# Kernel optimization log

Hardware: AMD Instinct MI355X
Metric: run time of the kernel (lower is better)

The kernel has to match this reference:

```python
import math
import jax, jax.numpy as jnp
import numpy as np

# Module config (init_kwargs)
GRID = (11, 16, 24)          # (T, H, W) latent grid, T odd so T-1 == 2*(T//2)
POOL = 128                   # pool_size / block size
SPARSITY = 0.9
TXT_LEN = 384                # txt_len, txt_first=False
HEADS, HDIM = 8, 128
FFL = GRID[1] * GRID[2]      # first_frame_len = H*W = 384
SEQ = GRID[0] * FFL + TXT_LEN  # 4608 tokens, 36 blocks of 128


def _rearr(t):
    # rearrange_with_remaining, h%8==0 and w%8==0 path.
    # t: [b, (f h w), n, d] with f = T-1 frames (first frame excluded)
    b, s, n, d = t.shape
    T, H, W = GRID
    fn, hn, wn = T // 2, H // 8, W // 8
    x = t.transpose(0, 2, 1, 3).reshape(b * n, fn, 2, hn, 8, wn, 8, d)
    # 'b (fn fb)(hn hb)(wn wb) d -> b (fn hn wn fb hb wb) d'
    x = x.transpose(0, 1, 3, 5, 2, 4, 6, 7).reshape(b * n, s, d)
    return x.reshape(b, n, s, d).transpose(0, 2, 1, 3)


def _inv_rearr(t):
    b, s, n, d = t.shape
    T, H, W = GRID
    fn, hn, wn = T // 2, H // 8, W // 8
    x = t.transpose(0, 2, 1, 3).reshape(b * n, fn, hn, wn, 2, 8, 8, d)
    x = x.transpose(0, 1, 4, 2, 5, 3, 6, 7).reshape(b * n, s, d)
    return x.reshape(b, n, s, d).transpose(0, 2, 1, 3)


def _avgpool(t):
    # seq divisible by POOL -> mean over each block (tail branch unused)
    b, s, n, d = t.shape
    return t.reshape(b, s // POOL, POOL, n, d).mean(axis=2)


def _forward(q, k, v):
    b, s, n, d = q.shape
    scale = jnp.asarray(d, q.dtype) ** -0.5
    # do_tensor_rearrange_pooling on concatenated qkv (txt_first=False)
    qkv = jnp.concatenate([q, k, v], axis=0)
    f_part = qkv[:, :FFL]
    i_part = qkv[:, FFL:s - TXT_LEN]
    t_part = qkv[:, s - TXT_LEN:]
    qkv2 = jnp.concatenate([_rearr(i_part), f_part, t_part], axis=1)
    pool = _avgpool(qkv2)
    q2, k2, v2 = jnp.split(qkv2, 3, axis=0)
    qp, kp, _ = jnp.split(pool, 3, axis=0)
    # pooled block scores + softmax
    ps = jax.nn.softmax(jnp.einsum('blnd,bsnd->bnls', qp, kp) * scale, axis=-1)
    nb = s // POOL
    keep = math.ceil(nb * (1.0 - SPARSITY))
    thr = jax.lax.top_k(ps, keep)[0][..., -1:]
    mask = ps >= thr                              # [B, n, nb, nb] bool
    prot = (FFL + TXT_LEN + POOL - 1) // POOL
    mask = mask.at[:, :, -prot:, :].set(True)
    mask = mask.at[:, :, :, -prot:].set(True)
    bm = mask[0]                                  # [n, nb, nb] per-head block mask (batch 0, as kernel uses)
    tok = jnp.repeat(jnp.repeat(bm, POOL, axis=1), POOL, axis=2)  # [n, S, S]
    # block-sparse attention == masked dense attention over selected kv blocks
    scores = jnp.einsum('bqnd,bknd->bnqk', q2, k2) * scale
    scores = jnp.where(tok[None], scores, jnp.asarray(-1e30, scores.dtype))
    p = jax.nn.softmax(scores, axis=-1)
    x = jnp.einsum('bnqk,bknd->bqnd', p, v2)
    # do_tensor_inv_rearrange (txt_first=False: concat(f, i, t))
    si = s - TXT_LEN - FFL
    xi = _inv_rearr(x[:, :si])
    xf = x[:, si:si + FFL]
    xt = x[:, si + FFL:]
    return jnp.concatenate([xf, xi, xt], axis=1)


def setup_inputs() -> dict:
    key = jax.random.key(0)
    kq, kk, kv = jax.random.split(key, 3)
    q = jax.random.normal(kq, (1, SEQ, HEADS, HDIM), dtype=jnp.float32)
    k = jax.random.normal(kk, (1, SEQ, HEADS, HDIM), dtype=jnp.float32)
    v = jax.random.normal(kv, (1, SEQ, HEADS, HDIM), dtype=jnp.float32)
    t_b_idx = jnp.arange(2, dtype=jnp.int64 if jax.config.jax_enable_x64 else jnp.int32)
    return {'q': q, 'k': k, 'v': v, 't_b_idx': t_b_idx}


def reference(q, k, v, t_b_idx):
    # t_idx = t_b_idx[0] = 0, skip_timesteps = 0 -> sparse branch (static)
    return _forward(q, k, v)
```

## Files before the change

kernel.cpp:

```cpp
#include <hip/hip_runtime.h>


typedef __attribute__((ext_vector_type(8))) _Float16 half8;
typedef __attribute__((ext_vector_type(4))) _Float16 half4;
typedef __attribute__((ext_vector_type(4))) float float4v;

#define KROW 136
#define VROW 72
#define PPROW 40

__device__ __forceinline__ int orig_pos(int j) {
    if (j >= 3840) return (j < 4224) ? (j - 3840) : j;
    int blk = j >> 7;
    int r   = j & 127;
    int f   = blk / 6;
    int rem = blk - f * 6;
    int b2  = rem / 3;
    int e   = rem - b2 * 3;
    int a   = r >> 6;
    int c   = (r >> 3) & 7;
    int g   = r & 7;
    return 384 + (f * 2 + a) * 384 + (b2 * 8 + c) * 24 + e * 8 + g;
}

__device__ __forceinline__ void cp16(const void* g, void* l) {
    __builtin_amdgcn_global_load_lds((const __attribute__((address_space(1))) void*)g,
                                     (__attribute__((address_space(3))) void*)l, 16, 0, 0);
}

__global__ __launch_bounds__(256) void prep_kernel(const float* __restrict__ q,
                                                   const float* __restrict__ k,
                                                   const float* __restrict__ v,
                                                   short* __restrict__ Kc,
                                                   unsigned* __restrict__ Vt32,
                                                   float* __restrict__ qp,
                                                   float* __restrict__ kp) {
    __shared__ short Vs[64 * KROW];
    __shared__ float Rs[8 * 128];
    int bx  = blockIdx.x;
    int tid = threadIdx.x;

    if (bx < 576) {
        int sub = bx & 1;
        int kb  = (bx >> 1) % 36;
        int h   = bx / 72;

        int lr = tid >> 3;
        int ld = (tid & 7) << 2;
#pragma unroll
        for (int pass = 0; pass < 2; ++pass) {
            int lt  = pass * 32 + lr;
            int tok = sub * 64 + lt;
            int op  = orig_pos(kb * 128 + tok);
            const float* kr = k + ((size_t)op * 8 + h) * 128;
            const float* vr = v + ((size_t)op * 8 + h) * 128;
            short* ko = Kc + ((size_t)(h * 36 + kb) * 128 + tok) * KROW;
#pragma unroll
            for (int j = 0; j < 4; ++j) {
                int d = ld + j * 32;
                float4v xk = *reinterpret_cast<const float4v*>(kr + d);
                float4v xv = *reinterpret_cast<const float4v*>(vr + d);
                half4 hk, hv;
#pragma unroll
                for (int i = 0; i < 4; ++i) { hk[i] = (_Float16)xk[i]; hv[i] = (_Float16)xv[i]; }
                *reinterpret_cast<half4*>(ko + d) = hk;
                *reinterpret_cast<half4*>(&Vs[lt * KROW + d]) = hv;
            }
        }
        __syncthreads();

        {
            const unsigned short* Vsu = (const unsigned short*)Vs;
            unsigned* vo = Vt32 + (size_t)((h * 36 + kb) * 2 + sub) * 128 * (VROW / 2);
#pragma unroll
            for (int it = 0; it < 16; ++it) {
                int i   = it * 256 + tid;
                int tw  = i & 31;
                int dim = i >> 5;
                unsigned lo = Vsu[(2 * tw) * KROW + dim];
                unsigned hi = Vsu[(2 * tw + 1) * KROW + dim];
                vo[dim * (VROW / 2) + tw] = (hi << 16) | lo;
            }
        }
    } else {
        int bx2 = bx - 576;
        int sub = bx2 & 1;
        int kb  = (bx2 >> 1) % 36;
        int h   = bx2 / 72;

        const float* arr = sub ? q : k;
        int dq = (tid & 31) << 2;
        int g  = tid >> 5;
        float4v acc = {0.f, 0.f, 0.f, 0.f};
#pragma unroll
        for (int it = 0; it < 16; ++it) {
            int t  = g + it * 8;
            int op = orig_pos(kb * 128 + t);
            float4v x = *reinterpret_cast<const float4v*>(arr + ((size_t)op * 8 + h) * 128 + dq);
            acc[0] += x[0]; acc[1] += x[1]; acc[2] += x[2]; acc[3] += x[3];
        }
#pragma unroll
        for (int i = 0; i < 4; ++i) Rs[g * 128 + dq + i] = acc[i];
        __syncthreads();

        if (tid < 128) {
            float s = 0.f;
#pragma unroll
            for (int g2 = 0; g2 < 8; ++g2) s += Rs[g2 * 128 + tid];
            float* outp = sub ? qp : kp;
            outp[(h * 36 + kb) * 128 + tid] = s * (1.f / 128.f);
        }
    }
}

__global__ __launch_bounds__(256, 3) void flash_kernel(const float* __restrict__ q,
                                                       const short* __restrict__ Kc,
                                                       const short* __restrict__ Vt,
                                                       const float* __restrict__ qp,
                                                       const float* __restrict__ kp,
                                                       float* __restrict__ out,
                                                       float* __restrict__ pO,
                                                       float* __restrict__ pL) {
    __shared__ __align__(16) short Ks[64 * KROW];
    __shared__ __align__(16) short Vsh[128 * VROW];
    __shared__ __align__(16) short Ph[4 * 32 * PPROW];
    __shared__ int Ls[40];
    __shared__ float Lf[64];

    int t = blockIdx.x;
    int h, qb, half, nkb = 0, kbase = 0, pidx = -1;
    if (t < 288) {
        h = t & 7;
        int rest = t >> 3;
        int qbh = rest / 6, r2 = rest % 6;
        half = r2 / 3;
        int chunk = r2 % 3;
        qb = 30 + qbh; nkb = 12; kbase = chunk * 12; pidx = t;
    } else {
        int t2 = t - 288;
        h = t2 & 7;
        int rest = t2 >> 3;
        qb = rest >> 1; half = rest & 1;
    }

    int tid = threadIdx.x, wave = tid >> 6, lane = tid & 63;
    int m16 = lane & 15, quad = lane >> 4;
    int rh = wave & 1, th = wave >> 1;

    constexpr float kScale = 0.08838834764831845f * 1.4426950408889634f;

    half8 aq[2][4];
#pragma unroll
    for (int rg = 0; rg < 2; ++rg) {
        int qrow_frag = qb * 128 + half * 64 + rh * 32 + rg * 16 + m16;
        const float* qrp = q + ((size_t)orig_pos(qrow_frag) * 8 + h) * 128;
#pragma unroll
        for (int kc = 0; kc < 4; ++kc) {
            float4v x0 = *reinterpret_cast<const float4v*>(qrp + kc * 32 + quad * 8);
            float4v x1 = *reinterpret_cast<const float4v*>(qrp + kc * 32 + quad * 8 + 4);
#pragma unroll
            for (int j = 0; j < 4; ++j) {
                aq[rg][kc][j]     = (_Float16)(x0[j] * kScale);
                aq[rg][kc][4 + j] = (_Float16)(x1[j] * kScale);
            }
        }
    }

    if (pidx < 0 && wave == 0) {
        float s = -1e30f;
        if (lane < 36) {
            const float4v* qv = (const float4v*)(qp + (h * 36 + qb) * 128);
            const float4v* kv = (const float4v*)(kp + (h * 36 + lane) * 128);
            float acc = 0.f;
            for (int i = 0; i < 32; ++i) {
                float4v a = qv[i], b = kv[i];
                acc += a[0] * b[0] + a[1] * b[1] + a[2] * b[2] + a[3] * b[3];
            }
            s = acc;
        }
        float tmp = s;
        float thr = 0.f;
        for (int i = 0; i < 4; ++i) {
            float mx = tmp;
            for (int off = 1; off < 64; off <<= 1) mx = fmaxf(mx, __shfl_xor(mx, off));
            thr = mx;
            unsigned long long bal = __ballot(tmp == mx);
            int low = __ffsll(bal) - 1;
            if (lane == low) tmp = -3e38f;
        }
        bool keep = (lane < 36) && ((s >= thr) || (lane >= 30));
        unsigned long long mk = __ballot(keep);
        if (lane == 0) Ls[0] = __popcll(mk);
        if (keep) {
            int pos = __popcll(mk & ((1ull << lane) - 1ull));
            Ls[1 + pos] = lane;
        }
    }
    __syncthreads();
    if (pidx < 0) nkb = Ls[0];

    float l_r[2][4];
    float4v o[2][8];
#pragma unroll
    for (int rg = 0; rg < 2; ++rg) {
#pragma unroll
        for (int r = 0; r < 4; ++r) l_r[rg][r] = 0.f;
#pragma unroll
        for (int dt = 0; dt < 8; ++dt) { o[rg][dt][0] = 0.f; o[rg][dt][1] = 0.f; o[rg][dt][2] = 0.f; o[rg][dt][3] = 0.f; }
    }

    short* Phw = Ph + wave * (32 * PPROW);

    int ntile = nkb * 2;
    for (int it = 0; it < ntile; ++it) {
        int kb  = (pidx >= 0) ? (kbase + (it >> 1)) : Ls[1 + (it >> 1)];
        int sub = it & 1;
        const char* gK = (const char*)(Kc + ((size_t)((h * 36 + kb) * 128) + sub * 64) * KROW);
        const char* gV = (const char*)(Vt + (size_t)((h * 36 + kb) * 2 + sub) * 128 * VROW);

        __syncthreads();
        {
            char* lK = (char*)Ks;
            char* lV = (char*)Vsh;
            int off = lane * 16;
            for (int c = wave; c < 35; c += 4) {
                if (c < 17) cp16(gK + c * 1024 + off, lK + c * 1024 + off);
                else        cp16(gV + (c - 17) * 1024 + off, lV + (c - 17) * 1024 + off);
            }
        }
        __syncthreads();

        float4v sacc[2][2];
#pragma unroll
        for (int rg = 0; rg < 2; ++rg)
#pragma unroll
            for (int nt = 0; nt < 2; ++nt) { sacc[rg][nt][0] = 0.f; sacc[rg][nt][1] = 0.f; sacc[rg][nt][2] = 0.f; sacc[rg][nt][3] = 0.f; }
#pragma unroll
        for (int nt = 0; nt < 2; ++nt)
#pragma unroll
            for (int kc = 0; kc < 4; ++kc) {
                half8 bk = *reinterpret_cast<const half8*>(&Ks[(th * 32 + nt * 16 + m16) * KROW + kc * 32 + quad * 8]);
                sacc[0][nt] = __builtin_amdgcn_mfma_f32_16x16x32_f16(aq[0][kc], bk, sacc[0][nt], 0, 0, 0);
                sacc[1][nt] = __builtin_amdgcn_mfma_f32_16x16x32_f16(aq[1][kc], bk, sacc[1][nt], 0, 0, 0);
            }

#pragma unroll
        for (int rg = 0; rg < 2; ++rg)
#pragma unroll
            for (int r = 0; r < 4; ++r) {
                float p0 = exp2f(sacc[rg][0][r]);
                float p1 = exp2f(sacc[rg][1][r]);
                sacc[rg][0][r] = p0; sacc[rg][1][r] = p1;
                l_r[rg][r] += p0 + p1;
            }

#pragma unroll
        for (int rg = 0; rg < 2; ++rg)
#pragma unroll
            for (int nt = 0; nt < 2; ++nt)
#pragma unroll
                for (int r = 0; r < 4; ++r) {
                    union { _Float16 hf; short s; } cv;
                    cv.hf = (_Float16)sacc[rg][nt][r];
                    Phw[(rg * 16 + quad * 4 + r) * PPROW + nt * 16 + m16] = cv.s;
                }
        half8 ap[2];
#pragma unroll
        for (int rg = 0; rg < 2; ++rg)
            ap[rg] = *reinterpret_cast<const half8*>(&Phw[(rg * 16 + m16) * PPROW + quad * 8]);

#pragma unroll
        for (int dt = 0; dt < 8; ++dt) {
            half8 bv = *reinterpret_cast<const half8*>(&Vsh[(dt * 16 + m16) * VROW + th * 32 + quad * 8]);
            o[0][dt] = __builtin_amdgcn_mfma_f32_16x16x32_f16(ap[0], bv, o[0][dt], 0, 0, 0);
            o[1][dt] = __builtin_amdgcn_mfma_f32_16x16x32_f16(ap[1], bv, o[1][dt], 0, 0, 0);
        }
    }

#pragma unroll
    for (int rg = 0; rg < 2; ++rg)
#pragma unroll
        for (int r = 0; r < 4; ++r)
            for (int sh = 1; sh < 16; sh <<= 1) l_r[rg][r] += __shfl_xor(l_r[rg][r], sh);

    __syncthreads();
    {
        float* red = rh ? (float*)Vsh : (float*)Ks;
        if (th == 1) {
#pragma unroll
            for (int rg = 0; rg < 2; ++rg) {
#pragma unroll
                for (int dt = 0; dt < 8; ++dt)
#pragma unroll
                    for (int r = 0; r < 4; ++r)
                        red[(rg * 16 + quad * 4 + r) * 132 + dt * 16 + m16] = o[rg][dt][r];
                if (m16 == 0)
#pragma unroll
                    for (int r = 0; r < 4; ++r)
                        Lf[rh * 32 + rg * 16 + quad * 4 + r] = l_r[rg][r];
            }
        }
        __syncthreads();
        if (th == 0) {
#pragma unroll
            for (int rg = 0; rg < 2; ++rg)
#pragma unroll
                for (int dt = 0; dt < 8; ++dt)
#pragma unroll
                    for (int r = 0; r < 4; ++r)
                        o[rg][dt][r] += red[(rg * 16 + quad * 4 + r) * 132 + dt * 16 + m16];

            if (pidx >= 0) {
                float* po = pO + (size_t)pidx * 8192;
#pragma unroll
                for (int rg = 0; rg < 2; ++rg)
#pragma unroll
                    for (int r = 0; r < 4; ++r) {
                        int row = rh * 32 + rg * 16 + quad * 4 + r;
                        float lt2 = l_r[rg][r] + Lf[row];
#pragma unroll
                        for (int dt = 0; dt < 8; ++dt)
                            po[row * 128 + dt * 16 + m16] = o[rg][dt][r];
                        if (m16 == 0) pL[pidx * 64 + row] = lt2;
                    }
            } else {
#pragma unroll
                for (int rg = 0; rg < 2; ++rg)
#pragma unroll
                    for (int r = 0; r < 4; ++r) {
                        int row = rh * 32 + rg * 16 + quad * 4 + r;
                        int qrow = qb * 128 + half * 64 + row;
                        size_t base = ((size_t)orig_pos(qrow) * 8 + h) * 128;
                        float inv = 1.f / (l_r[rg][r] + Lf[row]);
#pragma unroll
                        for (int dt = 0; dt < 8; ++dt)
                            out[base + dt * 16 + m16] = o[rg][dt][r] * inv;
                    }
            }
        }
    }
}

__global__ void combine_kernel(const float* __restrict__ pO, const float* __restrict__ pL,
                               float* __restrict__ out) {
    int gb = blockIdx.x;
    int g  = gb >> 3;
    int rg = gb & 7;
    int h    = g / 12;
    int rem  = g % 12;
    int qbh  = rem >> 1;
    int half = rem & 1;
    int qb   = 30 + qbh;
    int base_t = (qbh * 6 + half * 3) * 8 + h;

    int tid = threadIdx.x;
    int d   = tid & 127;
    int r0  = tid >> 7;
#pragma unroll
    for (int itr = 0; itr < 4; ++itr) {
        int row = rg * 8 + r0 + itr * 2;
        float l = pL[(base_t + 0) * 64 + row] + pL[(base_t + 8) * 64 + row] + pL[(base_t + 16) * 64 + row];
        float acc = pO[(size_t)(base_t + 0) * 8192 + row * 128 + d]
                  + pO[(size_t)(base_t + 8) * 8192 + row * 128 + d]
                  + pO[(size_t)(base_t + 16) * 8192 + row * 128 + d];
        int qrow = qb * 128 + half * 64 + row;
        out[((size_t)orig_pos(qrow) * 8 + h) * 128 + d] = acc / l;
    }
}

extern "C" void kernel_launch(void* const* d_in, const int* in_sizes, int n_in,
                              void* d_out, int out_size, void* d_ws, size_t ws_size,
                              hipStream_t stream) {
    const float* q = (const float*)d_in[0];
    const float* k = (const float*)d_in[1];
    const float* v = (const float*)d_in[2];
    float* out = (float*)d_out;

    char* w = (char*)d_ws;
    short* Kc  = (short*)(w);
    short* Vt  = (short*)(w + 10027008);
    float* qp  = (float*)(w + 20643840);
    float* kp  = (float*)(w + 20791296);
    float* pL  = (float*)(w + 20938752);
    float* pO  = (float*)(w + 21012480);

    prep_kernel<<<dim3(1152), dim3(256), 0, stream>>>(q, k, v, Kc, (unsigned*)Vt, qp, kp);
    flash_kernel<<<dim3(768), dim3(256), 0, stream>>>(q, Kc, Vt, qp, kp, out, pO, pL);
    combine_kernel<<<dim3(768), dim3(256), 0, stream>>>(pO, pL, out);
}
```

Measured before the change: 169.7 us.

## Fuse K pooling into K/V conversion kernel and split Q pooling out

The K block-mean is now accumulated while K is converted to fp16, so K is no longer re-read from global memory by separate pooling blocks. Per-half partial sums are written and summed inside the flash kernel's block-selection step. The fp16 K tile is now staged in LDS and written out with coalesced 16-byte stores, and the V staging row is padded to 138 to cut LDS bank conflicts on the transpose. Q pooling moves into its own kernel launch, adding one launch of overhead. The mean scaling is dropped, which leaves the scores scaled by a positive constant and so keeps the same ordering.

Result: no change. 172.4 us (+1.6%).

```diff
diff --git a/kernel.cpp b/kernel.cpp
--- a/kernel.cpp
+++ b/kernel.cpp
@@ -3,10 +3,12 @@
 
 typedef __attribute__((ext_vector_type(8))) _Float16 half8;
 typedef __attribute__((ext_vector_type(4))) _Float16 half4;
+typedef __attribute__((ext_vector_type(2))) _Float16 half2v;
 typedef __attribute__((ext_vector_type(4))) float float4v;
 
 #define KROW 136
 #define VROW 72
+#define VSROW 138
 #define PPROW 40
 
 __device__ __forceinline__ int orig_pos(int j) {
@@ -28,88 +30,112 @@
                                      (__attribute__((address_space(3))) void*)l, 16, 0, 0);
 }
 
-__global__ __launch_bounds__(256) void prep_kernel(const float* __restrict__ q,
-                                                   const float* __restrict__ k,
+__global__ __launch_bounds__(256) void conv_kernel(const float* __restrict__ k,
                                                    const float* __restrict__ v,
                                                    short* __restrict__ Kc,
                                                    unsigned* __restrict__ Vt32,
-                                                   float* __restrict__ qp,
-                                                   float* __restrict__ kp) {
-    __shared__ short Vs[64 * KROW];
+                                                   float* __restrict__ kpart) {
+    __shared__ __align__(16) short KsL[64 * KROW];
+    __shared__ short VsL[64 * VSROW];
+    __shared__ float Rs[32 * 128];
+    int bx  = blockIdx.x;
+    int tid = threadIdx.x;
+    int sub = bx & 1;
+    int kb  = (bx >> 1) % 36;
+    int h   = bx / 72;
+
+    int lr  = tid >> 3;
+    int ld4 = (tid & 7) << 2;
+
+    float ksum[16];
+#pragma unroll
+    for (int i = 0; i < 16; ++i) ksum[i] = 0.f;
+
+#pragma unroll
+    for (int pass = 0; pass < 2; ++pass) {
+        int lt  = pass * 32 + lr;
+        int tok = sub * 64 + lt;
+        int op  = orig_pos(kb * 128 + tok);
+        const float* kr = k + ((size_t)op * 8 + h) * 128;
+        const float* vr = v + ((size_t)op * 8 + h) * 128;
+#pragma unroll
+        for (int j = 0; j < 4; ++j) {
+            int d = ld4 + j * 32;
+            float4v xk = *reinterpret_cast<const float4v*>(kr + d);
+            float4v xv = *reinterpret_cast<const float4v*>(vr + d);
+            half4 hk;
+            half2v hv0, hv1;
+#pragma unroll
+            for (int i = 0; i < 4; ++i) { hk[i] = (_Float16)xk[i]; ksum[j * 4 + i] += xk[i]; }
+            hv0[0] = (_Float16)xv[0]; hv0[1] = (_Float16)xv[1];
+            hv1[0] = (_Float16)xv[2]; hv1[1] = (_Float16)xv[3];
+            *reinterpret_cast<half4*>(&KsL[lt * KROW + d]) = hk;
+            *reinterpret_cast<half2v*>(&VsL[lt * VSROW + d]) = hv0;
+            *reinterpret_cast<half2v*>(&VsL[lt * VSROW + d + 2]) = hv1;
+        }
+    }
+#pragma unroll
+    for (int j = 0; j < 4; ++j)
+#pragma unroll
+        for (int i = 0; i < 4; ++i)
+            Rs[lr * 128 + ld4 + j * 32 + i] = ksum[j * 4 + i];
+    __syncthreads();
+
+    {
+        const float4v* src = reinterpret_cast<const float4v*>(KsL);
+        float4v* dst = reinterpret_cast<float4v*>(Kc + ((size_t)((h * 36 + kb) * 128) + sub * 64) * KROW);
+        for (int i = tid; i < 1088; i += 256) dst[i] = src[i];
+    }
+
+    {
+        const unsigned short* Vsu = (const unsigned short*)VsL;
+        unsigned* vo = Vt32 + (size_t)((h * 36 + kb) * 2 + sub) * 128 * (VROW / 2);
+#pragma unroll
+        for (int it = 0; it < 16; ++it) {
+            int i   = it * 256 + tid;
+            int tw  = i & 31;
+            int dim = i >> 5;
+            unsigned lo = Vsu[(2 * tw) * VSROW + dim];
+            unsigned hi = Vsu[(2 * tw + 1) * VSROW + dim];
+            vo[dim * (VROW / 2) + tw] = (hi << 16) | lo;
+        }
+    }
+
+    if (tid < 128) {
+        float s = 0.f;
+#pragma unroll
+        for (int g = 0; g < 32; ++g) s += Rs[g * 128 + tid];
+        kpart[(size_t)((h * 36 + kb) * 2 + sub) * 128 + tid] = s;
+    }
+}
+
+__global__ __launch_bounds__(256) void poolq_kernel(const float* __restrict__ q,
+                                                    float* __restrict__ qp) {
     __shared__ float Rs[8 * 128];
     int bx  = blockIdx.x;
     int tid = threadIdx.x;
-
-    if (bx < 576) {
-        int sub = bx & 1;
-        int kb  = (bx >> 1) % 36;
-        int h   = bx / 72;
-
-        int lr = tid >> 3;
-        int ld = (tid & 7) << 2;
-#pragma unroll
-        for (int pass = 0; pass < 2; ++pass) {
-            int lt  = pass * 32 + lr;
-            int tok = sub * 64 + lt;
-            int op  = orig_pos(kb * 128 + tok);
-            const float* kr = k + ((size_t)op * 8 + h) * 128;
-            const float* vr = v + ((size_t)op * 8 + h) * 128;
-            short* ko = Kc + ((size_t)(h * 36 + kb) * 128 + tok) * KROW;
-#pragma unroll
-            for (int j = 0; j < 4; ++j) {
-                int d = ld + j * 32;
-                float4v xk = *reinterpret_cast<const float4v*>(kr + d);
-                float4v xv = *reinterpret_cast<const float4v*>(vr + d);
-                half4 hk, hv;
-#pragma unroll
-                for (int i = 0; i < 4; ++i) { hk[i] = (_Float16)xk[i]; hv[i] = (_Float16)xv[i]; }
-                *reinterpret_cast<half4*>(ko + d) = hk;
-                *reinterpret_cast<half4*>(&Vs[lt * KROW + d]) = hv;
-            }
-        }
-        __syncthreads();
-
-        {
-            const unsigned short* Vsu = (const unsigned short*)Vs;
-            unsigned* vo = Vt32 + (size_t)((h * 36 + kb) * 2 + sub) * 128 * (VROW / 2);
-#pragma unroll
-            for (int it = 0; it < 16; ++it) {
-                int i   = it * 256 + tid;
-                int tw  = i & 31;
-                int dim = i >> 5;
-                unsigned lo = Vsu[(2 * tw) * KROW + dim];
-                unsigned hi = Vsu[(2 * tw + 1) * KROW + dim];
-                vo[dim * (VROW / 2) + tw] = (hi << 16) | lo;
-            }
-        }
-    } else {
-        int bx2 = bx - 576;
-        int sub = bx2 & 1;
-        int kb  = (bx2 >> 1) % 36;
-        int h   = bx2 / 72;
-
-        const float* arr = sub ? q : k;
-        int dq = (tid & 31) << 2;
-        int g  = tid >> 5;
-        float4v acc = {0.f, 0.f, 0.f, 0.f};
-#pragma unroll
-        for (int it = 0; it < 16; ++it) {
-            int t  = g + it * 8;
-            int op = orig_pos(kb * 128 + t);
-            float4v x = *reinterpret_cast<const float4v*>(arr + ((size_t)op * 8 + h) * 128 + dq);
-            acc[0] += x[0]; acc[1] += x[1]; acc[2] += x[2]; acc[3] += x[3];
-        }
-#pragma unroll
-        for (int i = 0; i < 4; ++i) Rs[g * 128 + dq + i] = acc[i];
-        __syncthreads();
-
-        if (tid < 128) {
-            float s = 0.f;
-#pragma unroll
-            for (int g2 = 0; g2 < 8; ++g2) s += Rs[g2 * 128 + tid];
-            float* outp = sub ? qp : kp;
-            outp[(h * 36 + kb) * 128 + tid] = s * (1.f / 128.f);
-        }
+    int kb  = bx % 36;
+    int h   = bx / 36;
+
+    int dq = (tid & 31) << 2;
+    int g  = tid >> 5;
+    float4v acc = {0.f, 0.f, 0.f, 0.f};
+#pragma unroll
+    for (int it = 0; it < 16; ++it) {
+        int t  = g + it * 8;
+        int op = orig_pos(kb * 128 + t);
+        float4v x = *reinterpret_cast<const float4v*>(q + ((size_t)op * 8 + h) * 128 + dq);
+        acc[0] += x[0]; acc[1] += x[1]; acc[2] += x[2]; acc[3] += x[3];
+    }
+#pragma unroll
+    for (int i = 0; i < 4; ++i) Rs[g * 128 + dq + i] = acc[i];
+    __syncthreads();
+
+    if (tid < 128) {
+        float s = 0.f;
+#pragma unroll
+        for (int g2 = 0; g2 < 8; ++g2) s += Rs[g2 * 128 + tid];
+        qp[(h * 36 + kb) * 128 + tid] = s;
     }
 }
 
@@ -117,7 +143,7 @@
                                                        const short* __restrict__ Kc,
                                                        const short* __restrict__ Vt,
                                                        const float* __restrict__ qp,
-                                                       const float* __restrict__ kp,
+                                                       const float* __restrict__ kpart,
                                                        float* __restrict__ out,
                                                        float* __restrict__ pO,
                                                        float* __restrict__ pL) {
@@ -169,12 +195,14 @@
     if (pidx < 0 && wave == 0) {
         float s = -1e30f;
         if (lane < 36) {
-            const float4v* qv = (const float4v*)(qp + (h * 36 + qb) * 128);
-            const float4v* kv = (const float4v*)(kp + (h * 36 + lane) * 128);
+            const float4v* qv  = (const float4v*)(qp + (h * 36 + qb) * 128);
+            const float4v* kv0 = (const float4v*)(kpart + (size_t)((h * 36 + lane) * 2) * 128);
+            const float4v* kv1 = kv0 + 32;
             float acc = 0.f;
             for (int i = 0; i < 32; ++i) {
-                float4v a = qv[i], b = kv[i];
-                acc += a[0] * b[0] + a[1] * b[1] + a[2] * b[2] + a[3] * b[3];
+                float4v a = qv[i], b0 = kv0[i], b1 = kv1[i];
+                acc += a[0] * (b0[0] + b1[0]) + a[1] * (b0[1] + b1[1])
+                     + a[2] * (b0[2] + b1[2]) + a[3] * (b0[3] + b1[3]);
             }
             s = acc;
         }
@@ -377,14 +405,15 @@
     float* out = (float*)d_out;
 
     char* w = (char*)d_ws;
-    short* Kc  = (short*)(w);
-    short* Vt  = (short*)(w + 10027008);
-    float* qp  = (float*)(w + 20643840);
-    float* kp  = (float*)(w + 20791296);
-    float* pL  = (float*)(w + 20938752);
-    float* pO  = (float*)(w + 21012480);
-
-    prep_kernel<<<dim3(1152), dim3(256), 0, stream>>>(q, k, v, Kc, (unsigned*)Vt, qp, kp);
-    flash_kernel<<<dim3(768), dim3(256), 0, stream>>>(q, Kc, Vt, qp, kp, out, pO, pL);
+    short* Kc    = (short*)(w);
+    short* Vt    = (short*)(w + 10027008);
+    float* qp    = (float*)(w + 20643840);
+    float* kpart = (float*)(w + 20791296);
+    float* pL    = (float*)(w + 21086208);
+    float* pO    = (float*)(w + 21159936);
+
+    conv_kernel<<<dim3(576), dim3(256), 0, stream>>>(k, v, Kc, (unsigned*)Vt, kpart);
+    poolq_kernel<<<dim3(288), dim3(256), 0, stream>>>(q, qp);
+    flash_kernel<<<dim3(768), dim3(256), 0, stream>>>(q, Kc, Vt, qp, kpart, out, pO, pL);
     combine_kernel<<<dim3(768), dim3(256), 0, stream>>>(pO, pL, out);
 }
```

## Load K and V fragments directly from global memory instead of staging in LDS

Applied to the files above, without the earlier changes.

The flash kernel no longer copies each K/V tile into shared memory with async global-to-LDS loads and two barriers per tile. Each wave now reads its MFMA operand fragments straight from global (L2/L1-cached) memory, which removes the per-tile __syncthreads. A separate shared buffer is added for the final cross-wave reduction. The cost is redundant global traffic, since K/V rows are re-read by several waves, and exposed load latency with no prefetch.

Measured after the change: 175.1 us. +3.2%, slower.

```diff
diff --git a/kernel.cpp b/kernel.cpp
--- a/kernel.cpp
+++ b/kernel.cpp
@@ -23,11 +23,6 @@
     return 384 + (f * 2 + a) * 384 + (b2 * 8 + c) * 24 + e * 8 + g;
 }
 
-__device__ __forceinline__ void cp16(const void* g, void* l) {
-    __builtin_amdgcn_global_load_lds((const __attribute__((address_space(1))) void*)g,
-                                     (__attribute__((address_space(3))) void*)l, 16, 0, 0);
-}
-
 __global__ __launch_bounds__(256) void prep_kernel(const float* __restrict__ q,
                                                    const float* __restrict__ k,
                                                    const float* __restrict__ v,
@@ -121,9 +116,8 @@
                                                        float* __restrict__ out,
                                                        float* __restrict__ pO,
                                                        float* __restrict__ pL) {
-    __shared__ __align__(16) short Ks[64 * KROW];
-    __shared__ __align__(16) short Vsh[128 * VROW];
     __shared__ __align__(16) short Ph[4 * 32 * PPROW];
+    __shared__ __align__(16) float Red[2][32 * 132];
     __shared__ int Ls[40];
     __shared__ float Lf[64];
 
@@ -211,24 +205,15 @@
 
     short* Phw = Ph + wave * (32 * PPROW);
 
+    int kfo = (th * 32 + m16) * KROW + quad * 8;
+    int vfo = m16 * VROW + th * 32 + quad * 8;
+
     int ntile = nkb * 2;
     for (int it = 0; it < ntile; ++it) {
         int kb  = (pidx >= 0) ? (kbase + (it >> 1)) : Ls[1 + (it >> 1)];
         int sub = it & 1;
-        const char* gK = (const char*)(Kc + ((size_t)((h * 36 + kb) * 128) + sub * 64) * KROW);
-        const char* gV = (const char*)(Vt + (size_t)((h * 36 + kb) * 2 + sub) * 128 * VROW);
-
-        __syncthreads();
-        {
-            char* lK = (char*)Ks;
-            char* lV = (char*)Vsh;
-            int off = lane * 16;
-            for (int c = wave; c < 35; c += 4) {
-                if (c < 17) cp16(gK + c * 1024 + off, lK + c * 1024 + off);
-                else        cp16(gV + (c - 17) * 1024 + off, lV + (c - 17) * 1024 + off);
-            }
-        }
-        __syncthreads();
+        const short* gK = Kc + ((size_t)((h * 36 + kb) * 128) + sub * 64) * KROW;
+        const short* gV = Vt + (size_t)((h * 36 + kb) * 2 + sub) * 128 * VROW;
 
         float4v sacc[2][2];
 #pragma unroll
@@ -239,7 +224,7 @@
         for (int nt = 0; nt < 2; ++nt)
 #pragma unroll
             for (int kc = 0; kc < 4; ++kc) {
-                half8 bk = *reinterpret_cast<const half8*>(&Ks[(th * 32 + nt * 16 + m16) * KROW + kc * 32 + quad * 8]);
+                half8 bk = *reinterpret_cast<const half8*>(gK + kfo + nt * (16 * KROW) + kc * 32);
                 sacc[0][nt] = __builtin_amdgcn_mfma_f32_16x16x32_f16(aq[0][kc], bk, sacc[0][nt], 0, 0, 0);
                 sacc[1][nt] = __builtin_amdgcn_mfma_f32_16x16x32_f16(aq[1][kc], bk, sacc[1][nt], 0, 0, 0);
             }
@@ -271,7 +256,7 @@
 
 #pragma unroll
         for (int dt = 0; dt < 8; ++dt) {
-            half8 bv = *reinterpret_cast<const half8*>(&Vsh[(dt * 16 + m16) * VROW + th * 32 + quad * 8]);
+            half8 bv = *reinterpret_cast<const half8*>(gV + vfo + dt * (16 * VROW));
             o[0][dt] = __builtin_amdgcn_mfma_f32_16x16x32_f16(ap[0], bv, o[0][dt], 0, 0, 0);
             o[1][dt] = __builtin_amdgcn_mfma_f32_16x16x32_f16(ap[1], bv, o[1][dt], 0, 0, 0);
         }
@@ -285,7 +270,7 @@
 
     __syncthreads();
     {
-        float* red = rh ? (float*)Vsh : (float*)Ks;
+        float* red = &Red[rh][0];
         if (th == 1) {
 #pragma unroll
             for (int rg = 0; rg < 2; ++rg) {
```
